# Kernel optimization log

Measured on AMD Instinct MI355X. Metric: run time of the kernel, lower is better.

The kernel has to match this reference:

```python
import jax, jax.numpy as jnp
import numpy as np
import math

B, S, H = 2, 2048, 2048
NH, NKV, HD = 16, 8, 128          # heads, kv heads, head_dim
GROUPS = NH // NKV                 # 2
FF = 5632
EPS = 1e-6
SCALE = 0.02


def setup_inputs() -> dict:
    key = jax.random.key(0)
    ks = jax.random.split(key, 12)
    def w(k, shape):
        return jax.random.normal(k, shape, dtype=jnp.float32) * SCALE
    # additive causal mask: 0 on/below diagonal, -inf above
    causal = jnp.where(jnp.tril(jnp.ones((S, S), dtype=bool)), 0.0, -jnp.inf)
    attention_mask = causal[None, None].astype(jnp.float32)  # [1,1,S,S]
    return {
        "hidden_states": jax.random.normal(ks[0], (B, S, H), dtype=jnp.float32),
        "attention_mask": attention_mask,
        "q_w": w(ks[1], (NH * HD, H)),      # nn.Linear convention [out, in]
        "k_w": w(ks[2], (NKV * HD, H)),
        "v_w": w(ks[3], (NKV * HD, H)),
        "o_w": w(ks[4], (H, NH * HD)),
        "gate_w": w(ks[5], (FF, H)),
        "up_w": w(ks[6], (FF, H)),
        "down_w": w(ks[7], (H, FF)),
        "ln1_w": jnp.ones((H,), dtype=jnp.float32),
        "ln2_w": jnp.ones((H,), dtype=jnp.float32),
    }


def rmsnorm(x, w):
    var = jnp.mean(jnp.square(x), axis=-1, keepdims=True)
    return x * jax.lax.rsqrt(var + EPS) * w


def attention(x, mask, q_w, k_w, v_w, o_w):
    b, s, _ = x.shape
    q = (x @ q_w.T).reshape(b, s, NH, HD).transpose(0, 2, 1, 3)    # [b,nh,s,hd]
    k = (x @ k_w.T).reshape(b, s, NKV, HD).transpose(0, 2, 1, 3)   # [b,nkv,s,hd]
    v = (x @ v_w.T).reshape(b, s, NKV, HD).transpose(0, 2, 1, 3)
    # GQA: repeat_interleave kv heads to match query heads
    k = jnp.repeat(k, GROUPS, axis=1)
    v = jnp.repeat(v, GROUPS, axis=1)
    scores = jnp.einsum("bhqd,bhkd->bhqk", q, k) / math.sqrt(HD) + mask
    probs = jax.nn.softmax(scores.astype(jnp.float32), axis=-1).astype(q.dtype)
    out = jnp.einsum("bhqk,bhkd->bhqd", probs, v)
    out = out.transpose(0, 2, 1, 3).reshape(b, s, NH * HD)
    return out @ o_w.T


def mlp(x, gate_w, up_w, down_w):
    return (jax.nn.silu(x @ gate_w.T) * (x @ up_w.T)) @ down_w.T


def reference(hidden_states, attention_mask, q_w, k_w, v_w, o_w,
              gate_w, up_w, down_w, ln1_w, ln2_w):
    # pre-norm transformer layer with residuals
    h = hidden_states + attention(rmsnorm(hidden_states, ln1_w), attention_mask,
                                  q_w, k_w, v_w, o_w)
    out = h + mlp(rmsnorm(h, ln2_w), gate_w, up_w, down_w)
    return out
```

## Files before the change

### kernel.cpp

```cpp
#include <hip/hip_runtime.h>
#include <stdint.h>

typedef __bf16 bf16_t;
typedef __bf16 bf16x8 __attribute__((ext_vector_type(8)));
typedef __bf16 bf16x4 __attribute__((ext_vector_type(4)));
typedef float  f32x4  __attribute__((ext_vector_type(4)));

#define MFMA16(a, b, c) __builtin_amdgcn_mfma_f32_16x16x32_bf16((a), (b), (c), 0, 0, 0)

__device__ __forceinline__ void load_lds16(const bf16_t* g, bf16_t* l)
{
    __builtin_amdgcn_global_load_lds(
        (const __attribute__((address_space(1))) uint32_t*)(uintptr_t)g,
        (__attribute__((address_space(3))) uint32_t*)(uint32_t)(uintptr_t)l,
        16, 0, 0);
}

__device__ __forceinline__ void lds_stage2(const bf16_t* __restrict__ Gsrc,
                                           bf16_t* Ldst, int u0,
                                           int tid, int K, int k0)
{
#pragma unroll
    for (int l = 0; l < 2; ++l) {
        int u = u0 + l * 512 + tid;
        int row = u >> 3;
        int col = (((u & 7) ^ (row & 7)) << 3);
        load_lds16(Gsrc + (size_t)row * K + k0 + col, Ldst + u * 8);
    }
}

__global__ __launch_bounds__(256)
void wconv(const float* __restrict__ X, bf16_t* __restrict__ Y, int n)
{
    int i = (blockIdx.x * 256 + threadIdx.x) * 8;
    if (i >= n) return;
    f32x4 a = *(const f32x4*)(X + i);
    f32x4 b = *(const f32x4*)(X + i + 4);
    bf16x8 y;
#pragma unroll
    for (int e = 0; e < 4; ++e) { y[e] = (bf16_t)a[e]; y[e + 4] = (bf16_t)b[e]; }
    *(bf16x8*)(Y + i) = y;
}

__global__ __launch_bounds__(256)
void rmsnorm_f32(const float* __restrict__ X, const float* __restrict__ Wt,
                 bf16_t* __restrict__ Y)
{
    __shared__ float red[4];
    const int tid = threadIdx.x;
    const size_t row = blockIdx.x;
    const float* x = X + row * 2048;

    f32x4 x0 = *(const f32x4*)(x + tid * 8);
    f32x4 x1 = *(const f32x4*)(x + tid * 8 + 4);
    float ss = 0.f;
#pragma unroll
    for (int e = 0; e < 4; ++e) ss += x0[e] * x0[e] + x1[e] * x1[e];
#pragma unroll
    for (int off = 32; off; off >>= 1) ss += __shfl_xor(ss, off, 64);
    if ((tid & 63) == 0) red[tid >> 6] = ss;
    __syncthreads();
    float tot = red[0] + red[1] + red[2] + red[3];
    float scale = rsqrtf(tot * (1.f / 2048.f) + 1e-6f);

    f32x4 w0 = *(const f32x4*)(Wt + tid * 8);
    f32x4 w1 = *(const f32x4*)(Wt + tid * 8 + 4);
    bf16x8 yv;
#pragma unroll
    for (int e = 0; e < 4; ++e) {
        yv[e]     = (bf16_t)(x0[e] * scale * w0[e]);
        yv[e + 4] = (bf16_t)(x1[e] * scale * w1[e]);
    }
    *(bf16x8*)(Y + row * 2048 + tid * 8) = yv;
}

__global__ __launch_bounds__(256)
void rmsnorm_bf16(const bf16_t* __restrict__ X, const float* __restrict__ Wt,
                  bf16_t* __restrict__ Y)
{
    __shared__ float red[4];
    const int tid = threadIdx.x;
    const size_t row = blockIdx.x;

    bf16x8 xv = *(const bf16x8*)(X + row * 2048 + tid * 8);
    float xf[8];
    float ss = 0.f;
#pragma unroll
    for (int e = 0; e < 8; ++e) { xf[e] = (float)xv[e]; ss += xf[e] * xf[e]; }
#pragma unroll
    for (int off = 32; off; off >>= 1) ss += __shfl_xor(ss, off, 64);
    if ((tid & 63) == 0) red[tid >> 6] = ss;
    __syncthreads();
    float tot = red[0] + red[1] + red[2] + red[3];
    float scale = rsqrtf(tot * (1.f / 2048.f) + 1e-6f);

    f32x4 w0 = *(const f32x4*)(Wt + tid * 8);
    f32x4 w1 = *(const f32x4*)(Wt + tid * 8 + 4);
    bf16x8 yv;
#pragma unroll
    for (int e = 0; e < 4; ++e) {
        yv[e]     = (bf16_t)(xf[e] * scale * w0[e]);
        yv[e + 4] = (bf16_t)(xf[e + 4] * scale * w1[e]);
    }
    *(bf16x8*)(Y + row * 2048 + tid * 8) = yv;
}

__global__ __launch_bounds__(256, 2)
void gemm_bb(const bf16_t* __restrict__ A, const bf16_t* __restrict__ W,
             const float* __restrict__ Rf, const bf16_t* __restrict__ Rb,
             bf16_t* __restrict__ Cb, float* __restrict__ Cf,
             int M, int N, int K, int mode)
{
    __shared__ bf16_t As[128 * 64];
    __shared__ bf16_t Ws[128 * 64];

    const int tid  = threadIdx.x;
    const int lane = tid & 63, wave = tid >> 6;
    const int quad = lane >> 4, l16 = lane & 15;
    const int m0 = blockIdx.y * 128, n0 = blockIdx.x * 128;
    const int wm = (wave >> 1) * 64, wn = (wave & 1) * 64;

    const bf16_t* Ab = A + (size_t)(m0 + (tid >> 3)) * K + ((tid & 7) << 3);
    const bf16_t* Wb = W + (size_t)(n0 + (tid >> 3)) * K + ((tid & 7) << 3);

    f32x4 acc[4][4] = {};

    for (int k0 = 0; k0 < K; k0 += 64) {
        __syncthreads();
#pragma unroll
        for (int i = 0; i < 4; ++i) {
            load_lds16(Ab + (size_t)(i * 32) * K + k0, As + (i * 256 + tid) * 8);
            load_lds16(Wb + (size_t)(i * 32) * K + k0, Ws + (i * 256 + tid) * 8);
        }
        __syncthreads();

#pragma unroll
        for (int ks = 0; ks < 64; ks += 32) {
            bf16x8 af[4], bfr[4];
#pragma unroll
            for (int i = 0; i < 4; ++i)
                af[i] = *(const bf16x8*)(As + (wm + i * 16 + l16) * 64 + ks + quad * 8);
#pragma unroll
            for (int j = 0; j < 4; ++j)
                bfr[j] = *(const bf16x8*)(Ws + (wn + j * 16 + l16) * 64 + ks + quad * 8);
#pragma unroll
            for (int i = 0; i < 4; ++i)
#pragma unroll
                for (int j = 0; j < 4; ++j)
                    acc[i][j] = MFMA16(af[i], bfr[j], acc[i][j]);
        }
    }

#pragma unroll
    for (int i = 0; i < 4; ++i)
#pragma unroll
        for (int j = 0; j < 4; ++j)
#pragma unroll
            for (int r = 0; r < 4; ++r) {
                size_t row = (size_t)(m0 + wm + i * 16 + quad * 4 + r);
                size_t col = (size_t)(n0 + wn + j * 16 + l16);
                float v = acc[i][j][r];
                if (mode == 1) v += Rf[row * (size_t)N + col];
                if (mode == 2)
                    Cf[row * (size_t)N + col] = v + (float)Rb[row * (size_t)N + col];
                else
                    Cb[row * (size_t)N + col] = (bf16_t)v;
            }
}

__global__ __launch_bounds__(512, 2)
void gemm8(const bf16_t* __restrict__ A, const bf16_t* __restrict__ W,
           const float* __restrict__ Rf, const bf16_t* __restrict__ Rb,
           bf16_t* __restrict__ Cb, float* __restrict__ Cf,
           int M, int N, int K, int mode)
{
    __shared__ bf16_t As[2][256 * 64];
    __shared__ bf16_t Ws[2][128 * 64];

    const int tid  = threadIdx.x;
    const int lane = tid & 63, wave = tid >> 6;
    const int quad = lane >> 4, l16 = lane & 15;
    const int wr = wave >> 1, wc = wave & 1;

    const int lid = (int)blockIdx.x;
    const int swz = (lid & 7) * 32 + (lid >> 3);
    const int bym = swz >> 4;
    const int bxn = swz & 15;
    const int m0 = bym * 256, n0 = bxn * 128;

    const bf16_t* Ab = A + (size_t)m0 * K;
    const bf16_t* Wb = W + (size_t)n0 * K;

    const int xsw  = (l16 & 7) << 3;
    const int aoff = (wr * 64 + l16) * 64;
    const int boff = (wc * 64 + l16) * 64;

    f32x4 acc[4][4] = {};

    lds_stage2(Ab, As[0], 0,    tid, K, 0);
    lds_stage2(Ab, As[0], 1024, tid, K, 0);
    lds_stage2(Wb, Ws[0], 0,    tid, K, 0);

    const int NT = K >> 6;
    for (int t = 0; t < NT; ++t) {
        const int b  = t & 1;
        const int kn = (t + 1) << 6;
        const bool pf = (t + 1 < NT);
        bf16_t* An = As[1 - b];
        bf16_t* Wn = Ws[1 - b];

        if (pf) {
            lds_stage2(Ab, An, 0, tid, K, kn);
            asm volatile("s_waitcnt vmcnt(2)" ::: "memory");
        } else {
            asm volatile("s_waitcnt vmcnt(0)" ::: "memory");
        }
        __builtin_amdgcn_s_barrier();

        const bf16_t* Asb = As[b];
        const bf16_t* Wsb = Ws[b];

#pragma unroll
        for (int ks = 0; ks < 2; ++ks) {
            const int kxo = (ks * 32 + quad * 8) ^ xsw;
            bf16x8 af[4], bf_[4];
#pragma unroll
            for (int i = 0; i < 4; ++i)
                af[i] = *(const bf16x8*)(Asb + aoff + i * 1024 + kxo);
#pragma unroll
            for (int j = 0; j < 4; ++j)
                bf_[j] = *(const bf16x8*)(Wsb + boff + j * 1024 + kxo);
            if (pf) {
                if (ks == 0) lds_stage2(Ab, An, 1024, tid, K, kn);
                else         lds_stage2(Wb, Wn, 0,    tid, K, kn);
            }
            __builtin_amdgcn_s_barrier();
            __builtin_amdgcn_s_setprio(1);
#pragma unroll
            for (int i = 0; i < 4; ++i)
#pragma unroll
                for (int j = 0; j < 4; ++j)
                    acc[i][j] = MFMA16(af[i], bf_[j], acc[i][j]);
            __builtin_amdgcn_s_setprio(0);
            __builtin_amdgcn_s_barrier();
        }
    }

#pragma unroll
    for (int i = 0; i < 4; ++i)
#pragma unroll
        for (int j = 0; j < 4; ++j)
#pragma unroll
            for (int r = 0; r < 4; ++r) {
                size_t row = (size_t)(m0 + wr * 64 + i * 16 + quad * 4 + r);
                size_t col = (size_t)(n0 + wc * 64 + j * 16 + l16);
                float v = acc[i][j][r];
                if (mode == 1) v += Rf[row * (size_t)N + col];
                if (mode == 2)
                    Cf[row * (size_t)N + col] = v + (float)Rb[row * (size_t)N + col];
                else
                    Cb[row * (size_t)N + col] = (bf16_t)v;
            }
}

__global__ __launch_bounds__(512, 2)
void gateup8(const bf16_t* __restrict__ A, const bf16_t* __restrict__ G,
             const bf16_t* __restrict__ U, bf16_t* __restrict__ C,
             int M, int N, int K)
{
    __shared__ bf16_t As[2][256 * 64];
    __shared__ bf16_t Gs[2][128 * 64];
    __shared__ bf16_t Us[2][128 * 64];

    const int tid  = threadIdx.x;
    const int lane = tid & 63;
    const int wave = tid >> 6;
    const int quad = lane >> 4, l16 = lane & 15;
    const int wr = wave >> 2, wc = wave & 3;

    const int lid = (int)blockIdx.x;
    const int nwg = (M >> 8) * (N >> 7);
    const int cpx = nwg >> 3;
    const int swz = (lid & 7) * cpx + (lid >> 3);
    const int bxn = swz >> 4;
    const int bym = swz & 15;
    const int m0 = bym * 256, n0 = bxn * 128;

    const bf16_t* Ab = A + (size_t)m0 * K;
    const bf16_t* Gb = G + (size_t)n0 * K;
    const bf16_t* Ub = U + (size_t)n0 * K;

    const int xsw  = (l16 & 7) << 3;
    const int aoff = (wr * 128 + l16) * 64;
    const int boff = (wc * 32 + l16) * 64;

    f32x4 accg[8][2] = {};
    f32x4 accu[8][2] = {};

    lds_stage2(Ab, As[0], 0,    tid, K, 0);
    lds_stage2(Ab, As[0], 1024, tid, K, 0);
    lds_stage2(Gb, Gs[0], 0,    tid, K, 0);
    lds_stage2(Ub, Us[0], 0,    tid, K, 0);

    const int NT = K >> 6;
    for (int t = 0; t < NT; ++t) {
        const int b  = t & 1;
        const int kn = (t + 1) << 6;
        const bool pf = (t + 1 < NT);
        bf16_t* An = As[1 - b];
        bf16_t* Gn = Gs[1 - b];
        bf16_t* Un = Us[1 - b];

        if (pf) {
            lds_stage2(Ab, An, 0, tid, K, kn);
            asm volatile("s_waitcnt vmcnt(2)" ::: "memory");
        } else {
            asm volatile("s_waitcnt vmcnt(0)" ::: "memory");
        }
        __builtin_amdgcn_s_barrier();

        const bf16_t* Asb = As[b];
        const bf16_t* Gsb = Gs[b];
        const bf16_t* Usb = Us[b];

        bf16x8 af[4], bg[2], bu[2];

        {
            const int kxo = (quad * 8) ^ xsw;
#pragma unroll
            for (int i = 0; i < 4; ++i)
                af[i] = *(const bf16x8*)(Asb + aoff + i * 1024 + kxo);
#pragma unroll
            for (int j = 0; j < 2; ++j) {
                bg[j] = *(const bf16x8*)(Gsb + boff + j * 1024 + kxo);
                bu[j] = *(const bf16x8*)(Usb + boff + j * 1024 + kxo);
            }
        }
        if (pf) lds_stage2(Ab, An, 1024, tid, K, kn);
        __builtin_amdgcn_s_barrier();
        __builtin_amdgcn_s_setprio(1);
#pragma unroll
        for (int i = 0; i < 4; ++i)
#pragma unroll
            for (int j = 0; j < 2; ++j) {
                accg[i][j] = MFMA16(af[i], bg[j], accg[i][j]);
                accu[i][j] = MFMA16(af[i], bu[j], accu[i][j]);
            }
        __builtin_amdgcn_s_setprio(0);
        __builtin_amdgcn_s_barrier();

        {
            const int kxo = (quad * 8) ^ xsw;
#pragma unroll
            for (int i = 0; i < 4; ++i)
                af[i] = *(const bf16x8*)(Asb + aoff + (i + 4) * 1024 + kxo);
        }
        if (pf) lds_stage2(Gb, Gn, 0, tid, K, kn);
        __builtin_amdgcn_s_barrier();
        __builtin_amdgcn_s_setprio(1);
#pragma unroll
        for (int i = 0; i < 4; ++i)
#pragma unroll
            for (int j = 0; j < 2; ++j) {
                accg[i + 4][j] = MFMA16(af[i], bg[j], accg[i + 4][j]);
                accu[i + 4][j] = MFMA16(af[i], bu[j], accu[i + 4][j]);
            }
        __builtin_amdgcn_s_setprio(0);
        __builtin_amdgcn_s_barrier();

        {
            const int kxo = (32 + quad * 8) ^ xsw;
#pragma unroll
            for (int i = 0; i < 4; ++i)
                af[i] = *(const bf16x8*)(Asb + aoff + i * 1024 + kxo);
#pragma unroll
            for (int j = 0; j < 2; ++j) {
                bg[j] = *(const bf16x8*)(Gsb + boff + j * 1024 + kxo);
                bu[j] = *(const bf16x8*)(Usb + boff + j * 1024 + kxo);
            }
        }
        if (pf) lds_stage2(Ub, Un, 0, tid, K, kn);
        __builtin_amdgcn_s_barrier();
        __builtin_amdgcn_s_setprio(1);
#pragma unroll
        for (int i = 0; i < 4; ++i)
#pragma unroll
            for (int j = 0; j < 2; ++j) {
                accg[i][j] = MFMA16(af[i], bg[j], accg[i][j]);
                accu[i][j] = MFMA16(af[i], bu[j], accu[i][j]);
            }
        __builtin_amdgcn_s_setprio(0);
        __builtin_amdgcn_s_barrier();

        {
            const int kxo = (32 + quad * 8) ^ xsw;
#pragma unroll
            for (int i = 0; i < 4; ++i)
                af[i] = *(const bf16x8*)(Asb + aoff + (i + 4) * 1024 + kxo);
        }
        __builtin_amdgcn_s_barrier();
        __builtin_amdgcn_s_setprio(1);
#pragma unroll
        for (int i = 0; i < 4; ++i)
#pragma unroll
            for (int j = 0; j < 2; ++j) {
                accg[i + 4][j] = MFMA16(af[i], bg[j], accg[i + 4][j]);
                accu[i + 4][j] = MFMA16(af[i], bu[j], accu[i + 4][j]);
            }
        __builtin_amdgcn_s_setprio(0);
        __builtin_amdgcn_s_barrier();
    }

#pragma unroll
    for (int i = 0; i < 8; ++i)
#pragma unroll
        for (int j = 0; j < 2; ++j)
#pragma unroll
            for (int r = 0; r < 4; ++r) {
                size_t row = (size_t)(m0 + wr * 128 + i * 16 + quad * 4 + r);
                size_t col = (size_t)(n0 + wc * 32 + j * 16 + l16);
                float g = accg[i][j][r];
                float u = accu[i][j][r];
                float sig = 1.f / (1.f + __expf(fminf(-g, 80.f)));
                C[row * (size_t)N + col] = (bf16_t)(g * sig * u);
            }
}

__global__ __launch_bounds__(256, 2)
void gemm_bt(const bf16_t* __restrict__ A, const float* __restrict__ W,
             const float* __restrict__ Rf, const bf16_t* __restrict__ Rb,
             bf16_t* __restrict__ Cb, float* __restrict__ Cf,
             int M, int N, int K, int mode)
{
    __shared__ bf16_t As[128 * 64];
    __shared__ bf16_t Ws[128 * 64];

    const int tid  = threadIdx.x;
    const int lane = tid & 63, wave = tid >> 6;
    const int quad = lane >> 4, l16 = lane & 15;
    const int m0 = blockIdx.y * 128, n0 = blockIdx.x * 128;
    const int wm = (wave >> 1) * 64, wn = (wave & 1) * 64;

    f32x4 acc[4][4] = {};

    for (int k0 = 0; k0 < K; k0 += 64) {
        bf16x8 ra[4];
        bf16x4 rw[8];
#pragma unroll
        for (int i = 0; i < 4; ++i) {
            int u = i * 256 + tid;
            int r = u >> 3, c = (u & 7) << 3;
            ra[i] = *(const bf16x8*)(A + (size_t)(m0 + r) * K + k0 + c);
        }
#pragma unroll
        for (int i = 0; i < 8; ++i) {
            int u = i * 256 + tid;
            int r = u >> 4, c = (u & 15) << 2;
            f32x4 w4 = *(const f32x4*)(W + (size_t)(n0 + r) * K + k0 + c);
#pragma unroll
            for (int e = 0; e < 4; ++e) rw[i][e] = (bf16_t)w4[e];
        }
        __syncthreads();
#pragma unroll
        for (int i = 0; i < 4; ++i)
            *(bf16x8*)(As + (i * 256 + tid) * 8) = ra[i];
#pragma unroll
        for (int i = 0; i < 8; ++i)
            *(bf16x4*)(Ws + (i * 256 + tid) * 4) = rw[i];
        __syncthreads();

#pragma unroll
        for (int ks = 0; ks < 64; ks += 32) {
            bf16x8 af[4], bfr[4];
#pragma unroll
            for (int i = 0; i < 4; ++i)
                af[i] = *(const bf16x8*)(As + (wm + i * 16 + l16) * 64 + ks + quad * 8);
#pragma unroll
            for (int j = 0; j < 4; ++j)
                bfr[j] = *(const bf16x8*)(Ws + (wn + j * 16 + l16) * 64 + ks + quad * 8);
#pragma unroll
            for (int i = 0; i < 4; ++i)
#pragma unroll
                for (int j = 0; j < 4; ++j)
                    acc[i][j] = MFMA16(af[i], bfr[j], acc[i][j]);
        }
    }

#pragma unroll
    for (int i = 0; i < 4; ++i)
#pragma unroll
        for (int j = 0; j < 4; ++j)
#pragma unroll
            for (int r = 0; r < 4; ++r) {
                size_t row = (size_t)(m0 + wm + i * 16 + quad * 4 + r);
                size_t col = (size_t)(n0 + wn + j * 16 + l16);
                float v = acc[i][j][r];
                if (mode == 1) v += Rf[row * (size_t)N + col];
                if (mode == 2)
                    Cf[row * (size_t)N + col] = v + (float)Rb[row * (size_t)N + col];
                else
                    Cb[row * (size_t)N + col] = (bf16_t)v;
            }
}

__global__ __launch_bounds__(256, 2)
void gemm_gateup(const bf16_t* __restrict__ A, const float* __restrict__ G,
                 const float* __restrict__ U, bf16_t* __restrict__ C,
                 int M, int N, int K)
{
    __shared__ bf16_t As[128 * 64];
    __shared__ bf16_t Gs[128 * 64];
    __shared__ bf16_t Us[128 * 64];

    const int tid  = threadIdx.x;
    const int lane = tid & 63, wave = tid >> 6;
    const int quad = lane >> 4, l16 = lane & 15;
    const int m0 = blockIdx.y * 128, n0 = blockIdx.x * 128;
    const int wm = (wave >> 1) * 64, wn = (wave & 1) * 64;

    f32x4 accg[4][4] = {};
    f32x4 accu[4][4] = {};

    for (int k0 = 0; k0 < K; k0 += 64) {
        bf16x8 ra[4];
        bf16x4 rg[8], ru[8];
#pragma unroll
        for (int i = 0; i < 4; ++i) {
            int u = i * 256 + tid;
            int r = u >> 3, c = (u & 7) << 3;
            ra[i] = *(const bf16x8*)(A + (size_t)(m0 + r) * K + k0 + c);
        }
#pragma unroll
        for (int i = 0; i < 8; ++i) {
            int u = i * 256 + tid;
            int r = u >> 4, c = (u & 15) << 2;
            f32x4 g4 = *(const f32x4*)(G + (size_t)(n0 + r) * K + k0 + c);
            f32x4 u4 = *(const f32x4*)(U + (size_t)(n0 + r) * K + k0 + c);
#pragma unroll
            for (int e = 0; e < 4; ++e) { rg[i][e] = (bf16_t)g4[e]; ru[i][e] = (bf16_t)u4[e]; }
        }
        __syncthreads();
#pragma unroll
        for (int i = 0; i < 4; ++i)
            *(bf16x8*)(As + (i * 256 + tid) * 8) = ra[i];
#pragma unroll
        for (int i = 0; i < 8; ++i) {
            *(bf16x4*)(Gs + (i * 256 + tid) * 4) = rg[i];
            *(bf16x4*)(Us + (i * 256 + tid) * 4) = ru[i];
        }
        __syncthreads();

#pragma unroll
        for (int ks = 0; ks < 64; ks += 32) {
            bf16x8 af[4], bg[4], bu[4];
#pragma unroll
            for (int i = 0; i < 4; ++i)
                af[i] = *(const bf16x8*)(As + (wm + i * 16 + l16) * 64 + ks + quad * 8);
#pragma unroll
            for (int j = 0; j < 4; ++j) {
                bg[j] = *(const bf16x8*)(Gs + (wn + j * 16 + l16) * 64 + ks + quad * 8);
                bu[j] = *(const bf16x8*)(Us + (wn + j * 16 + l16) * 64 + ks + quad * 8);
            }
#pragma unroll
            for (int i = 0; i < 4; ++i)
#pragma unroll
                for (int j = 0; j < 4; ++j) {
                    accg[i][j] = MFMA16(af[i], bg[j], accg[i][j]);
                    accu[i][j] = MFMA16(af[i], bu[j], accu[i][j]);
                }
        }
    }

#pragma unroll
    for (int i = 0; i < 4; ++i)
#pragma unroll
        for (int j = 0; j < 4; ++j)
#pragma unroll
            for (int r = 0; r < 4; ++r) {
                size_t row = (size_t)(m0 + wm + i * 16 + quad * 4 + r);
                size_t col = (size_t)(n0 + wn + j * 16 + l16);
                float g = accg[i][j][r];
                float u = accu[i][j][r];
                float sig = 1.f / (1.f + __expf(fminf(-g, 80.f)));
                C[row * (size_t)N + col] = (bf16_t)(g * sig * u);
            }
}

__global__ __launch_bounds__(256, 2)
void attn_fwd(const bf16_t* __restrict__ Q, const bf16_t* __restrict__ Kg,
              const bf16_t* __restrict__ Vg, bf16_t* __restrict__ O)
{
    __shared__ bf16_t Ks[64 * 128];
    __shared__ bf16_t Vt[128 * 64];
    __shared__ bf16_t Pl[4][16 * 72];

    const int tid  = threadIdx.x;
    const int lane = tid & 63, wave = tid >> 6;
    const int quad = lane >> 4, l16 = lane & 15;
    const int bh = blockIdx.y, b = bh >> 4, h = bh & 15;

    const bf16_t* Qh = Q  + (size_t)b * 2048 * 2048 + (size_t)h * 128;
    const bf16_t* Kh = Kg + (size_t)b * 2048 * 1024 + (size_t)(h >> 1) * 128;
    const bf16_t* Vh = Vg + (size_t)b * 2048 * 1024 + (size_t)(h >> 1) * 128;

    const float scale = 0.08838834764831845f;

#pragma unroll 1
    for (int pass = 0; pass < 2; ++pass) {
        const int qt = pass ? (31 - (int)blockIdx.x) : (int)blockIdx.x;
        const int q0 = qt * 64;

        bf16x8 aq[4];
#pragma unroll
        for (int ks = 0; ks < 4; ++ks)
            aq[ks] = *(const bf16x8*)(Qh + (size_t)(q0 + wave * 16 + l16) * 2048 + ks * 32 + quad * 8);

        float m_r[4] = { -30000.f, -30000.f, -30000.f, -30000.f };
        float l_r[4] = { 0.f, 0.f, 0.f, 0.f };
        f32x4 acc_o[8] = {};

        const int ntiles = qt + 1;

        for (int t = 0; t < ntiles; ++t) {
            const int kv0 = t * 64;
            __syncthreads();
#pragma unroll
            for (int i = 0; i < 4; ++i) {
                int u = i * 256 + tid;
                int rk = u >> 4, c = (u & 15) << 3;
                *(bf16x8*)(Ks + u * 8) =
                    *(const bf16x8*)(Kh + (size_t)(kv0 + rk) * 1024 + c);
            }
#pragma unroll
            for (int it = 0; it < 4; ++it) {
                int v = it * 256 + tid;
                int d = v & 127, kb = v >> 7;
                bf16x8 vt8;
#pragma unroll
                for (int j = 0; j < 8; ++j)
                    vt8[j] = Vh[(size_t)(kv0 + kb * 8 + j) * 1024 + d];
                *(bf16x8*)(Vt + d * 64 + ((kb ^ (d & 7)) << 3)) = vt8;
            }
            __syncthreads();

            f32x4 accs[4] = {};
#pragma unroll
            for (int ks = 0; ks < 4; ++ks)
#pragma unroll
                for (int j = 0; j < 4; ++j) {
                    bf16x8 bk = *(const bf16x8*)(Ks + (j * 16 + l16) * 128 + ks * 32 + quad * 8);
                    accs[j] = MFMA16(aq[ks], bk, accs[j]);
                }

#pragma unroll
            for (int r = 0; r < 4; ++r) {
                const int qrow = q0 + wave * 16 + quad * 4 + r;
                float s[4];
                float mx = -30000.f;
#pragma unroll
                for (int j = 0; j < 4; ++j) {
                    s[j] = accs[j][r] * scale;
                    if (kv0 + j * 16 + l16 > qrow) s[j] = -30000.f;
                    mx = fmaxf(mx, s[j]);
                }
                mx = fmaxf(mx, __shfl_xor(mx, 1, 64));
                mx = fmaxf(mx, __shfl_xor(mx, 2, 64));
                mx = fmaxf(mx, __shfl_xor(mx, 4, 64));
                mx = fmaxf(mx, __shfl_xor(mx, 8, 64));
                float mnew  = fmaxf(m_r[r], mx);
                float alpha = __expf(fmaxf(m_r[r] - mnew, -80.f));
                float rs = 0.f;
#pragma unroll
                for (int j = 0; j < 4; ++j) {
                    float p = __expf(fmaxf(s[j] - mnew, -80.f));
                    rs += p;
                    Pl[wave][(quad * 4 + r) * 72 + j * 16 + l16] = (bf16_t)p;
                }
                rs += __shfl_xor(rs, 1, 64);
                rs += __shfl_xor(rs, 2, 64);
                rs += __shfl_xor(rs, 4, 64);
                rs += __shfl_xor(rs, 8, 64);
                l_r[r] = l_r[r] * alpha + rs;
                m_r[r] = mnew;
#pragma unroll
                for (int nt = 0; nt < 8; ++nt) acc_o[nt][r] *= alpha;
            }

            __syncthreads();

#pragma unroll
            for (int ks2 = 0; ks2 < 2; ++ks2) {
                bf16x8 ap = *(const bf16x8*)(&Pl[wave][l16 * 72 + ks2 * 32 + quad * 8]);
                const int kb_r = ks2 * 4 + quad;
#pragma unroll
                for (int nt = 0; nt < 8; ++nt) {
                    const int d = nt * 16 + l16;
                    bf16x8 bv = *(const bf16x8*)(Vt + d * 64 + ((kb_r ^ (d & 7)) << 3));
                    acc_o[nt] = MFMA16(ap, bv, acc_o[nt]);
                }
            }
        }

#pragma unroll
        for (int r = 0; r < 4; ++r) {
            float inv = 1.f / fmaxf(l_r[r], 1e-30f);
            size_t orow = (size_t)b * 2048 + q0 + wave * 16 + quad * 4 + r;
#pragma unroll
            for (int nt = 0; nt < 8; ++nt)
                O[orow * 2048 + h * 128 + nt * 16 + l16] = (bf16_t)(acc_o[nt][r] * inv);
        }
    }
}

extern "C" void kernel_launch(void* const* d_in, const int* in_sizes, int n_in,
                              void* d_out, int out_size, void* d_ws, size_t ws_size,
                              hipStream_t stream)
{
    const float* x   = (const float*)d_in[0];
    const float* qw  = (const float*)d_in[2];
    const float* kw  = (const float*)d_in[3];
    const float* vw  = (const float*)d_in[4];
    const float* ow  = (const float*)d_in[5];
    const float* gw  = (const float*)d_in[6];
    const float* uw  = (const float*)d_in[7];
    const float* dw  = (const float*)d_in[8];
    const float* ln1 = (const float*)d_in[9];
    const float* ln2 = (const float*)d_in[10];
    float*  out = (float*)d_out;
    bf16_t* ws  = (bf16_t*)d_ws;

    dim3 blk(256);
    const size_t NEED = 87031808ull * 2;

    if (ws_size >= NEED) {
        bf16_t* wq = ws;
        bf16_t* wk = ws + 4194304;
        bf16_t* wv = ws + 6291456;
        bf16_t* wo = ws + 8388608;
        bf16_t* wg = ws + 12582912;
        bf16_t* wu = ws + 24117248;
        bf16_t* wd = ws + 35651584;
        bf16_t* h1 = ws + 47185920;
        bf16_t* qb = ws + 55574528;
        bf16_t* kb = ws + 63963136;
        bf16_t* vb = ws + 68157440;
        bf16_t* ab = (bf16_t*)d_out;
        bf16_t* hb = qb;
        bf16_t* gb = kb;

        wconv<<<2048, blk, 0, stream>>>(qw, wq, 4194304);
        wconv<<<1024, blk, 0, stream>>>(kw, wk, 2097152);
        wconv<<<1024, blk, 0, stream>>>(vw, wv, 2097152);
        wconv<<<2048, blk, 0, stream>>>(ow, wo, 4194304);
        wconv<<<5632, blk, 0, stream>>>(gw, wg, 11534336);
        wconv<<<5632, blk, 0, stream>>>(uw, wu, 11534336);
        wconv<<<5632, blk, 0, stream>>>(dw, wd, 11534336);

        rmsnorm_f32<<<4096, blk, 0, stream>>>(x, ln1, h1);
        gemm8<<<256, dim3(512), 0, stream>>>(h1, wq, nullptr, nullptr, qb, nullptr, 4096, 2048, 2048, 0);
        gemm_bb<<<dim3( 8, 32), blk, 0, stream>>>(h1, wk, nullptr, nullptr, kb, nullptr, 4096, 1024, 2048, 0);
        gemm_bb<<<dim3( 8, 32), blk, 0, stream>>>(h1, wv, nullptr, nullptr, vb, nullptr, 4096, 1024, 2048, 0);
        attn_fwd<<<dim3(16, 32), blk, 0, stream>>>(qb, kb, vb, ab);
        gemm8<<<256, dim3(512), 0, stream>>>(ab, wo, x, nullptr, hb, nullptr, 4096, 2048, 2048, 1);
        rmsnorm_bf16<<<4096, blk, 0, stream>>>(hb, ln2, h1);
        gateup8<<<704, dim3(512), 0, stream>>>(h1, wg, wu, gb, 4096, 5632, 2048);
        gemm8<<<256, dim3(512), 0, stream>>>(gb, wd, nullptr, hb, nullptr, out, 4096, 2048, 5632, 2);
    } else {
        const size_t ME = 1ull << 20;
        bf16_t* h1 = ws;
        bf16_t* qb = ws + 8  * ME;
        bf16_t* kb = ws + 16 * ME;
        bf16_t* vb = ws + 20 * ME;
        bf16_t* ab = (bf16_t*)d_out;
        bf16_t* hb = ws + 8  * ME;
        bf16_t* gb = ws + 16 * ME;

        rmsnorm_f32<<<4096, blk, 0, stream>>>(x, ln1, h1);
        gemm_bt<<<dim3(16, 32), blk, 0, stream>>>(h1, qw, nullptr, nullptr, qb, nullptr, 4096, 2048, 2048, 0);
        gemm_bt<<<dim3( 8, 32), blk, 0, stream>>>(h1, kw, nullptr, nullptr, kb, nullptr, 4096, 1024, 2048, 0);
        gemm_bt<<<dim3( 8, 32), blk, 0, stream>>>(h1, vw, nullptr, nullptr, vb, nullptr, 4096, 1024, 2048, 0);
        attn_fwd<<<dim3(16, 32), blk, 0, stream>>>(qb, kb, vb, ab);
        gemm_bt<<<dim3(16, 32), blk, 0, stream>>>(ab, ow, x, nullptr, hb, nullptr, 4096, 2048, 2048, 1);
        rmsnorm_bf16<<<4096, blk, 0, stream>>>(hb, ln2, h1);
        gemm_gateup<<<dim3(44, 32), blk, 0, stream>>>(h1, gw, uw, gb, 4096, 5632, 2048);
        gemm_bt<<<dim3(16, 32), blk, 0, stream>>>(gb, dw, nullptr, hb, nullptr, out, 4096, 2048, 5632, 2);
    }
}
```

Measured before the change: 887.2 us.

## Fuse K/V projections into one gemm8 and split gate/up with fused SiLU epilogue

Computes K and V with a single gemm8 call over the contiguous wk/wv weights, writing an interleaved KV buffer that attention reads with a stride of 2048. The gate/up projection is replaced by two gemm8 launches: the gate result goes to an extra workspace buffer and is applied as silu(g)*u in the up GEMM's epilogue. The tile swizzle is generalized to arbitrary N-tile counts and now walks M-tiles fastest. This needs a larger workspace and adds a round trip of the gate intermediate through memory.

```diff
diff --git a/kernel.cpp b/kernel.cpp
--- a/kernel.cpp
+++ b/kernel.cpp
@@ -172,7 +172,7 @@
 void gemm8(const bf16_t* __restrict__ A, const bf16_t* __restrict__ W,
            const float* __restrict__ Rf, const bf16_t* __restrict__ Rb,
            bf16_t* __restrict__ Cb, float* __restrict__ Cf,
-           int M, int N, int K, int mode)
+           int M, int N, int K, int nbx, int mode)
 {
     __shared__ bf16_t As[2][256 * 64];
     __shared__ bf16_t Ws[2][128 * 64];
@@ -183,9 +183,11 @@
     const int wr = wave >> 1, wc = wave & 1;
 
     const int lid = (int)blockIdx.x;
-    const int swz = (lid & 7) * 32 + (lid >> 3);
-    const int bym = swz >> 4;
-    const int bxn = swz & 15;
+    const int nwg = (M >> 8) * nbx;
+    const int q   = nwg >> 3;
+    const int swz = (lid & 7) * q + (lid >> 3);
+    const int bxn = swz >> 4;
+    const int bym = swz & 15;
     const int m0 = bym * 256, n0 = bxn * 128;
 
     const bf16_t* Ab = A + (size_t)m0 * K;
@@ -256,6 +258,11 @@
                 size_t col = (size_t)(n0 + wc * 64 + j * 16 + l16);
                 float v = acc[i][j][r];
                 if (mode == 1) v += Rf[row * (size_t)N + col];
+                if (mode == 4) {
+                    float g = (float)Rb[row * (size_t)N + col];
+                    float sig = 1.f / (1.f + __expf(fminf(-g, 80.f)));
+                    v *= g * sig;
+                }
                 if (mode == 2)
                     Cf[row * (size_t)N + col] = v + (float)Rb[row * (size_t)N + col];
                 else
@@ -588,7 +595,7 @@
 
 __global__ __launch_bounds__(256, 2)
 void attn_fwd(const bf16_t* __restrict__ Q, const bf16_t* __restrict__ Kg,
-              const bf16_t* __restrict__ Vg, bf16_t* __restrict__ O)
+              const bf16_t* __restrict__ Vg, bf16_t* __restrict__ O, int kvs)
 {
     __shared__ bf16_t Ks[64 * 128];
     __shared__ bf16_t Vt[128 * 64];
@@ -600,8 +607,8 @@
     const int bh = blockIdx.y, b = bh >> 4, h = bh & 15;
 
     const bf16_t* Qh = Q  + (size_t)b * 2048 * 2048 + (size_t)h * 128;
-    const bf16_t* Kh = Kg + (size_t)b * 2048 * 1024 + (size_t)(h >> 1) * 128;
-    const bf16_t* Vh = Vg + (size_t)b * 2048 * 1024 + (size_t)(h >> 1) * 128;
+    const bf16_t* Kh = Kg + (size_t)b * 2048 * kvs + (size_t)(h >> 1) * 128;
+    const bf16_t* Vh = Vg + (size_t)b * 2048 * kvs + (size_t)(h >> 1) * 128;
 
     const float scale = 0.08838834764831845f;
 
@@ -629,7 +636,7 @@
                 int u = i * 256 + tid;
                 int rk = u >> 4, c = (u & 15) << 3;
                 *(bf16x8*)(Ks + u * 8) =
-                    *(const bf16x8*)(Kh + (size_t)(kv0 + rk) * 1024 + c);
+                    *(const bf16x8*)(Kh + (size_t)(kv0 + rk) * kvs + c);
             }
 #pragma unroll
             for (int it = 0; it < 4; ++it) {
@@ -638,7 +645,7 @@
                 bf16x8 vt8;
 #pragma unroll
                 for (int j = 0; j < 8; ++j)
-                    vt8[j] = Vh[(size_t)(kv0 + kb * 8 + j) * 1024 + d];
+                    vt8[j] = Vh[(size_t)(kv0 + kb * 8 + j) * kvs + d];
                 *(bf16x8*)(Vt + d * 64 + ((kb ^ (d & 7)) << 3)) = vt8;
             }
             __syncthreads();
@@ -730,9 +737,10 @@
     bf16_t* ws  = (bf16_t*)d_ws;
 
     dim3 blk(256);
-    const size_t NEED = 87031808ull * 2;
-
-    if (ws_size >= NEED) {
+    const size_t NEED1 = 87031808ull * 2;
+    const size_t NEED2 = (87031808ull + 23068672ull) * 2;
+
+    if (ws_size >= NEED1) {
         bf16_t* wq = ws;
         bf16_t* wk = ws + 4194304;
         bf16_t* wv = ws + 6291456;
@@ -747,6 +755,7 @@
         bf16_t* ab = (bf16_t*)d_out;
         bf16_t* hb = qb;
         bf16_t* gb = kb;
+        bf16_t* gr = ws + 87031808;
 
         wconv<<<2048, blk, 0, stream>>>(qw, wq, 4194304);
         wconv<<<1024, blk, 0, stream>>>(kw, wk, 2097152);
@@ -757,14 +766,27 @@
         wconv<<<5632, blk, 0, stream>>>(dw, wd, 11534336);
 
         rmsnorm_f32<<<4096, blk, 0, stream>>>(x, ln1, h1);
-        gemm8<<<256, dim3(512), 0, stream>>>(h1, wq, nullptr, nullptr, qb, nullptr, 4096, 2048, 2048, 0);
-        gemm_bb<<<dim3( 8, 32), blk, 0, stream>>>(h1, wk, nullptr, nullptr, kb, nullptr, 4096, 1024, 2048, 0);
-        gemm_bb<<<dim3( 8, 32), blk, 0, stream>>>(h1, wv, nullptr, nullptr, vb, nullptr, 4096, 1024, 2048, 0);
-        attn_fwd<<<dim3(16, 32), blk, 0, stream>>>(qb, kb, vb, ab);
-        gemm8<<<256, dim3(512), 0, stream>>>(ab, wo, x, nullptr, hb, nullptr, 4096, 2048, 2048, 1);
-        rmsnorm_bf16<<<4096, blk, 0, stream>>>(hb, ln2, h1);
-        gateup8<<<704, dim3(512), 0, stream>>>(h1, wg, wu, gb, 4096, 5632, 2048);
-        gemm8<<<256, dim3(512), 0, stream>>>(gb, wd, nullptr, hb, nullptr, out, 4096, 2048, 5632, 2);
+
+        if (ws_size >= NEED2) {
+            bf16_t* kv = kb;
+            gemm8<<<256, dim3(512), 0, stream>>>(h1, wq, nullptr, nullptr, qb, nullptr, 4096, 2048, 2048, 16, 0);
+            gemm8<<<256, dim3(512), 0, stream>>>(h1, wk, nullptr, nullptr, kv, nullptr, 4096, 2048, 2048, 16, 0);
+            attn_fwd<<<dim3(16, 32), blk, 0, stream>>>(qb, kv, kv + 1024, ab, 2048);
+            gemm8<<<256, dim3(512), 0, stream>>>(ab, wo, x, nullptr, hb, nullptr, 4096, 2048, 2048, 16, 1);
+            rmsnorm_bf16<<<4096, blk, 0, stream>>>(hb, ln2, h1);
+            gemm8<<<704, dim3(512), 0, stream>>>(h1, wg, nullptr, nullptr, gr, nullptr, 4096, 5632, 2048, 44, 0);
+            gemm8<<<704, dim3(512), 0, stream>>>(h1, wu, nullptr, gr, gb, nullptr, 4096, 5632, 2048, 44, 4);
+            gemm8<<<256, dim3(512), 0, stream>>>(gb, wd, nullptr, hb, nullptr, out, 4096, 2048, 5632, 16, 2);
+        } else {
+            gemm8<<<256, dim3(512), 0, stream>>>(h1, wq, nullptr, nullptr, qb, nullptr, 4096, 2048, 2048, 16, 0);
+            gemm_bb<<<dim3( 8, 32), blk, 0, stream>>>(h1, wk, nullptr, nullptr, kb, nullptr, 4096, 1024, 2048, 0);
+            gemm_bb<<<dim3( 8, 32), blk, 0, stream>>>(h1, wv, nullptr, nullptr, vb, nullptr, 4096, 1024, 2048, 0);
+            attn_fwd<<<dim3(16, 32), blk, 0, stream>>>(qb, kb, vb, ab, 1024);
+            gemm8<<<256, dim3(512), 0, stream>>>(ab, wo, x, nullptr, hb, nullptr, 4096, 2048, 2048, 16, 1);
+            rmsnorm_bf16<<<4096, blk, 0, stream>>>(hb, ln2, h1);
+            gateup8<<<704, dim3(512), 0, stream>>>(h1, wg, wu, gb, 4096, 5632, 2048);
+            gemm8<<<256, dim3(512), 0, stream>>>(gb, wd, nullptr, hb, nullptr, out, 4096, 2048, 5632, 16, 2);
+        }
     } else {
         const size_t ME = 1ull << 20;
         bf16_t* h1 = ws;
@@ -779,7 +801,7 @@
         gemm_bt<<<dim3(16, 32), blk, 0, stream>>>(h1, qw, nullptr, nullptr, qb, nullptr, 4096, 2048, 2048, 0);
         gemm_bt<<<dim3( 8, 32), blk, 0, stream>>>(h1, kw, nullptr, nullptr, kb, nullptr, 4096, 1024, 2048, 0);
         gemm_bt<<<dim3( 8, 32), blk, 0, stream>>>(h1, vw, nullptr, nullptr, vb, nullptr, 4096, 1024, 2048, 0);
-        attn_fwd<<<dim3(16, 32), blk, 0, stream>>>(qb, kb, vb, ab);
+        attn_fwd<<<dim3(16, 32), blk, 0, stream>>>(qb, kb, vb, ab, 1024);
         gemm_bt<<<dim3(16, 32), blk, 0, stream>>>(ab, ow, x, nullptr, hb, nullptr, 4096, 2048, 2048, 1);
         rmsnorm_bf16<<<4096, blk, 0, stream>>>(hb, ln2, h1);
         gemm_gateup<<<dim3(44, 32), blk, 0, stream>>>(h1, gw, uw, gb, 4096, 5632, 2048);
```

Result: slower. 1.060 ms (+19.5%).
